# Kernel optimization log

Measured on AMD Instinct MI355X. Metric: run time of the kernel, lower is better.

The kernel has to match this reference:

```python
import jax, jax.numpy as jnp
import numpy as np

H = 512     # LSTM_HIDDEN_SIZE
IN = 64     # LSTM_INPUT_SIZE
B = 256
T = 512
OUT = 96    # output_size (decode horizon)


def setup_inputs() -> dict:
    key = jax.random.key(0)
    ks = jax.random.split(key, 32)
    k = 1.0 / np.sqrt(H)
    u = lambda kk, shape: jax.random.uniform(kk, shape, jnp.float32, -k, k)
    inp = {"inputs": jax.random.normal(ks[0], (B, T, IN), jnp.float32)}
    shapes = {
        "enc_Wih0": (4 * H, IN), "enc_Whh0": (4 * H, H), "enc_bih0": (4 * H,), "enc_bhh0": (4 * H,),
        "enc_Wih1": (4 * H, H),  "enc_Whh1": (4 * H, H), "enc_bih1": (4 * H,), "enc_bhh1": (4 * H,),
        "dec_Wih0": (4 * H, 1),  "dec_Whh0": (4 * H, H), "dec_bih0": (4 * H,), "dec_bhh0": (4 * H,),
        "dec_Wih1": (4 * H, H),  "dec_Whh1": (4 * H, H), "dec_bih1": (4 * H,), "dec_bhh1": (4 * H,),
        "proj_W": (1, H), "proj_b": (1,),
    }
    for i, (name, sh) in enumerate(shapes.items()):
        inp[name] = u(ks[i + 1], sh)
    inp["output_size"] = OUT
    return inp


def lstm_cell(x, h, c, Wih, Whh, bih, bhh):
    # PyTorch gate order: i, f, g, o
    z = x @ Wih.T + h @ Whh.T + (bih + bhh)
    i, f, g, o = jnp.split(z, 4, axis=-1)
    c_new = jax.nn.sigmoid(f) * c + jax.nn.sigmoid(i) * jnp.tanh(g)
    h_new = jax.nn.sigmoid(o) * jnp.tanh(c_new)
    return h_new, c_new


def reference(inputs,
              enc_Wih0, enc_Whh0, enc_bih0, enc_bhh0,
              enc_Wih1, enc_Whh1, enc_bih1, enc_bhh1,
              dec_Wih0, dec_Whh0, dec_bih0, dec_bhh0,
              dec_Wih1, dec_Whh1, dec_bih1, dec_bhh1,
              proj_W, proj_b, output_size):
    bsz = inputs.shape[0]
    hdim = enc_Whh0.shape[1]
    z = jnp.zeros((bsz, hdim), inputs.dtype)

    # ---- encoder: 2-layer LSTM over time (batch_first -> time-major scan) ----
    def enc_step(carry, x_t):
        h0, c0, h1, c1 = carry
        h0, c0 = lstm_cell(x_t, h0, c0, enc_Wih0, enc_Whh0, enc_bih0, enc_bhh0)
        h1, c1 = lstm_cell(h0, h1, c1, enc_Wih1, enc_Whh1, enc_bih1, enc_bhh1)
        return (h0, c0, h1, c1), None

    xs = jnp.swapaxes(inputs, 0, 1)  # [T, B, IN]
    (h0, c0, h1, c1), _ = jax.lax.scan(enc_step, (z, z, z, z), xs)

    def dec_step(carry, _):
        h0, c0, h1, c1, x = carry  # x: [B, 1]
        h0, c0 = lstm_cell(x, h0, c0, dec_Wih0, dec_Whh0, dec_bih0, dec_bhh0)
        h1, c1 = lstm_cell(h0, h1, c1, dec_Wih1, dec_Whh1, dec_bih1, dec_bhh1)
        y = h1 @ proj_W.T + proj_b  # [B, 1]
        return (h0, c0, h1, c1, y), y

    x0 = jnp.zeros((bsz, 1), inputs.dtype)
    _, ys = jax.lax.scan(dec_step, (h0, c0, h1, c1, x0), None, length=output_size)
    # ys: [OUT, B, 1] -> [B, OUT, 1]
    return jnp.swapaxes(ys, 0, 1)
```

## Files before the change

kernel.cpp:

```cpp
#include <hip/hip_runtime.h>
#include <math.h>

#define Bb   256
#define Tt   512
#define INn  64
#define Hh   512
#define OUTn 96
#define TPB  512
#define SP   (Hh*Bb)
#define RSTRIDE 36
#define HDR  12288

struct Params {
  const float *Xt;
  float *H0, *H1;
  unsigned int *flags;
  unsigned int *rel;
  const float *Wih0,*Whh0,*bih0,*bhh0,*Wih1,*Whh1,*bih1,*bhh1;
  const float *dWih0,*dWhh0,*dbih0,*dbhh0,*dWih1,*dWhh1,*dbih1,*dbhh1;
  const float *projW,*projb;
  float *out;
};

__device__ __forceinline__ float sigm(float x){ return 1.0f/(1.0f + expf(-x)); }

__device__ __forceinline__ void gridbar(unsigned int* flags, unsigned int* rel,
                                        unsigned int g, int nwg) {
  __syncthreads();
  const int tid = threadIdx.x;
  if (blockIdx.x == 0) {
    if (tid > 0 && tid < nwg) {
      while (__hip_atomic_load(&flags[tid*16], __ATOMIC_RELAXED, __HIP_MEMORY_SCOPE_AGENT) < g)
        __builtin_amdgcn_s_sleep(1);
    }
    __syncthreads();
    if (tid == 0) {
      __threadfence();
      __hip_atomic_store(rel, g, __ATOMIC_RELEASE, __HIP_MEMORY_SCOPE_AGENT);
    }
    __syncthreads();
  } else {
    if (tid == 0) {
      __threadfence();
      __hip_atomic_store(&flags[blockIdx.x*16], g, __ATOMIC_RELEASE, __HIP_MEMORY_SCOPE_AGENT);
      while (__hip_atomic_load(rel, __ATOMIC_RELAXED, __HIP_MEMORY_SCOPE_AGENT) < g)
        __builtin_amdgcn_s_sleep(1);
      __threadfence();
    }
    __syncthreads();
  }
}

__global__ void __launch_bounds__(256) xpose(const float* __restrict__ X, float* __restrict__ Xt) {
  __shared__ float tile[64][65];
  const int t = blockIdx.x;
  const int l = threadIdx.x & 63;
  const int r = threadIdx.x >> 6;
  for (int qd = 0; qd < 4; ++qd) {
    #pragma unroll
    for (int rep = 0; rep < 16; ++rep) {
      int bl = rep*4 + r;
      tile[bl][l] = X[(size_t)(qd*64 + bl)*(Tt*INn) + (size_t)t*INn + l];
    }
    __syncthreads();
    #pragma unroll
    for (int rep = 0; rep < 16; ++rep) {
      int i = rep*4 + r;
      Xt[(size_t)t*(INn*Bb) + (size_t)i*Bb + qd*64 + l] = tile[l][i];
    }
    __syncthreads();
  }
}

#define BFLY4(a)                                                   \
  do { _Pragma("unroll")                                           \
    for (int m_ = 0; m_ < 4; ++m_) {                               \
      a[m_] += __shfl_xor(a[m_], 8, 64);                           \
      a[m_] += __shfl_xor(a[m_], 16, 64);                          \
      a[m_] += __shfl_xor(a[m_], 32, 64);                          \
    } } while (0)

__global__ void __launch_bounds__(TPB, 4) lstm512(Params P) {
  __shared__ float WA[512][20];
  __shared__ float WB[512][8];
  __shared__ float WX[64][8];
  __shared__ float BS[16];
  __shared__ float PW[Hh];
  __shared__ float WXD[8];
  __shared__ float PBs;

  const int tid  = threadIdx.x;
  const int lane = tid & 63;
  const int kh   = lane >> 3;
  const int bqlo = lane & 7;
  const int bqhi = (tid >> 6) & 3;
  const int h    = tid >> 8;
  const int bq   = bqhi*8 + bqlo;
  const int uw   = blockIdx.x >> 1;
  const int bh   = blockIdx.x & 1;
  const int j    = 2*uw + h;
  const int h8   = h*8, h4 = h*4;
  const int boff = 128*bh + 4*bq;
  unsigned int bgen = 1;

  for (int e = tid; e < 512*16; e += TPB) {
    int k = e >> 4, c = e & 15, hh = c >> 3, s = c & 7;
    int unit = 2*uw + hh;
    WA[k][c] = (s < 4) ? P.Wih1[(size_t)(s*Hh + unit)*Hh + k]
                       : P.Whh0[(size_t)((s-4)*Hh + unit)*Hh + k];
  }
  for (int e = tid; e < 512*8; e += TPB) {
    int k = e >> 3, c = e & 7, hh = c >> 2, g = c & 3;
    WB[k][c] = P.Whh1[(size_t)(g*Hh + 2*uw + hh)*Hh + k];
  }
  for (int e = tid; e < 64*8; e += TPB) {
    int k = e >> 3, c = e & 7, hh = c >> 2, g = c & 3;
    WX[k][c] = P.Wih0[(size_t)(g*Hh + 2*uw + hh)*INn + k];
  }
  if (tid < 16) {
    int c = tid, hh = c >> 3, s = c & 7;
    int unit = 2*uw + hh;
    BS[c] = (s < 4) ? (P.bih1[s*Hh+unit] + P.bhh1[s*Hh+unit])
                    : (P.bih0[(s-4)*Hh+unit] + P.bhh0[(s-4)*Hh+unit]);
  }
  __syncthreads();

  float c0[4] = {0,0,0,0}, c1[4] = {0,0,0,0};

  for (int p = -1; p <= 511; ++p) {
    float z1i[4], z1f[4], z1g[4], z1o[4];
    float z0i[4], z0f[4], z0g[4], z0o[4];
    #pragma unroll
    for (int m = 0; m < 4; ++m) {
      z1i[m] = (kh==0) ? BS[h8+0] : 0.f; z1f[m] = (kh==0) ? BS[h8+1] : 0.f;
      z1g[m] = (kh==0) ? BS[h8+2] : 0.f; z1o[m] = (kh==0) ? BS[h8+3] : 0.f;
      z0i[m] = (kh==0) ? BS[h8+4] : 0.f; z0f[m] = (kh==0) ? BS[h8+5] : 0.f;
      z0g[m] = (kh==0) ? BS[h8+6] : 0.f; z0o[m] = (kh==0) ? BS[h8+7] : 0.f;
    }
    const float* __restrict__ h0in = P.H0 + (size_t)(p & 1)*SP + boff;
    const float* __restrict__ h1in = P.H1 + (size_t)((p+1) & 1)*SP + boff;
    #pragma unroll 4
    for (int kk = 0; kk < 64; ++kk) {
      const int k = kk*8 + kh;
      const float4 w1 = *reinterpret_cast<const float4*>(&WA[k][h8]);
      const float4 w0 = *reinterpret_cast<const float4*>(&WA[k][h8+4]);
      const float4 wb = *reinterpret_cast<const float4*>(&WB[k][h4]);
      const float4 hv4 = *reinterpret_cast<const float4*>(&h0in[k*Bb]);
      const float4 gv4 = *reinterpret_cast<const float4*>(&h1in[k*Bb]);
      const float* hv = &hv4.x;
      const float* gv = &gv4.x;
      #pragma unroll
      for (int m = 0; m < 4; ++m) {
        z1i[m]=fmaf(w1.x,hv[m],z1i[m]); z1f[m]=fmaf(w1.y,hv[m],z1f[m]);
        z1g[m]=fmaf(w1.z,hv[m],z1g[m]); z1o[m]=fmaf(w1.w,hv[m],z1o[m]);
        z0i[m]=fmaf(w0.x,hv[m],z0i[m]); z0f[m]=fmaf(w0.y,hv[m],z0f[m]);
        z0g[m]=fmaf(w0.z,hv[m],z0g[m]); z0o[m]=fmaf(w0.w,hv[m],z0o[m]);
        z1i[m]=fmaf(wb.x,gv[m],z1i[m]); z1f[m]=fmaf(wb.y,gv[m],z1f[m]);
        z1g[m]=fmaf(wb.z,gv[m],z1g[m]); z1o[m]=fmaf(wb.w,gv[m],z1o[m]);
      }
    }
    {
      int tx = (p+1 < Tt) ? (p+1) : (Tt-1);
      const float* __restrict__ xin = P.Xt + (size_t)tx*(INn*Bb) + boff;
      #pragma unroll
      for (int kk = 0; kk < 8; ++kk) {
        const int k = kk*8 + kh;
        const float4 wv = *reinterpret_cast<const float4*>(&WX[k][h4]);
        const float4 xv4 = *reinterpret_cast<const float4*>(&xin[k*Bb]);
        const float* xv = &xv4.x;
        #pragma unroll
        for (int m = 0; m < 4; ++m) {
          z0i[m]=fmaf(wv.x,xv[m],z0i[m]); z0f[m]=fmaf(wv.y,xv[m],z0f[m]);
          z0g[m]=fmaf(wv.z,xv[m],z0g[m]); z0o[m]=fmaf(wv.w,xv[m],z0o[m]);
        }
      }
    }
    BFLY4(z1i); BFLY4(z1f); BFLY4(z1g); BFLY4(z1o);
    BFLY4(z0i); BFLY4(z0f); BFLY4(z0g); BFLY4(z0o);

    if (p >= 0) {
      float4 o; float* ov = &o.x;
      #pragma unroll
      for (int m = 0; m < 4; ++m) {
        c1[m] = sigm(z1f[m])*c1[m] + sigm(z1i[m])*tanhf(z1g[m]);
        ov[m] = sigm(z1o[m])*tanhf(c1[m]);
      }
      if (kh == 0)
        *reinterpret_cast<float4*>(P.H1 + (size_t)(p & 1)*SP + (size_t)j*Bb + boff) = o;
    }
    if (p < 511) {
      float4 o; float* ov = &o.x;
      #pragma unroll
      for (int m = 0; m < 4; ++m) {
        c0[m] = sigm(z0f[m])*c0[m] + sigm(z0i[m])*tanhf(z0o[m]*0.f + z0g[m]);
        ov[m] = sigm(z0o[m])*tanhf(c0[m]);
      }
      if (kh == 0)
        *reinterpret_cast<float4*>(P.H0 + (size_t)((p+1) & 1)*SP + (size_t)j*Bb + boff) = o;
    }
    gridbar(P.flags, P.rel, bgen, 512); ++bgen;
  }

  for (int e = tid; e < 512*16; e += TPB) {
    int k = e >> 4, c = e & 15, hh = c >> 3, s = c & 7;
    int unit = 2*uw + hh;
    WA[k][c] = (s < 4) ? P.dWih1[(size_t)(s*Hh + unit)*Hh + k]
                       : P.dWhh1[(size_t)((s-4)*Hh + unit)*Hh + k];
  }
  for (int e = tid; e < 512*8; e += TPB) {
    int k = e >> 3, c = e & 7, hh = c >> 2, g = c & 3;
    WB[k][c] = P.dWhh0[(size_t)(g*Hh + 2*uw + hh)*Hh + k];
  }
  if (tid < 8) {
    int c = tid, hh = c >> 2, g = c & 3;
    WXD[c] = P.dWih0[g*Hh + 2*uw + hh];
  }
  if (tid >= 16 && tid < 32) {
    int c = tid - 16, hh = c >> 3, s = c & 7;
    int unit = 2*uw + hh;
    BS[c] = (s < 4) ? (P.dbih1[s*Hh+unit] + P.dbhh1[s*Hh+unit])
                    : (P.dbih0[(s-4)*Hh+unit] + P.dbhh0[(s-4)*Hh+unit]);
  }
  for (int k = tid; k < Hh; k += TPB) PW[k] = P.projW[k];
  if (tid == 0) PBs = P.projb[0];
  __syncthreads();

  for (int q = 0; q < OUTn; ++q) {
    float xq[4] = {0,0,0,0};
    if (q > 0) {
      const float* __restrict__ h1p = P.H1 + (size_t)((q+1)&1)*SP + boff;
      float acc[4] = {0,0,0,0};
      #pragma unroll 4
      for (int kk = 0; kk < 64; ++kk) {
        const int k = kk*8 + kh;
        float pw = PW[k];
        const float4 hp4 = *reinterpret_cast<const float4*>(&h1p[k*Bb]);
        const float* hp = &hp4.x;
        #pragma unroll
        for (int m = 0; m < 4; ++m) acc[m] = fmaf(pw, hp[m], acc[m]);
      }
      BFLY4(acc);
      #pragma unroll
      for (int m = 0; m < 4; ++m) xq[m] = acc[m] + PBs;
      if (uw == 0 && h == 0 && kh == 0) {
        #pragma unroll
        for (int m = 0; m < 4; ++m) P.out[(size_t)(boff + m)*OUTn + (q-1)] = xq[m];
      }
    }
    float zdi[4], zdf[4], zdg[4], zdo[4];
    #pragma unroll
    for (int m = 0; m < 4; ++m) {
      zdi[m] = (kh==0) ? BS[h8+4] : 0.f; zdf[m] = (kh==0) ? BS[h8+5] : 0.f;
      zdg[m] = (kh==0) ? BS[h8+6] : 0.f; zdo[m] = (kh==0) ? BS[h8+7] : 0.f;
    }
    {
      const float* __restrict__ h0p = P.H0 + (size_t)((q+1)&1)*SP + boff;
      #pragma unroll 4
      for (int kk = 0; kk < 64; ++kk) {
        const int k = kk*8 + kh;
        const float4 wv = *reinterpret_cast<const float4*>(&WB[k][h4]);
        const float4 hv4 = *reinterpret_cast<const float4*>(&h0p[k*Bb]);
        const float* hv = &hv4.x;
        #pragma unroll
        for (int m = 0; m < 4; ++m) {
          zdi[m]=fmaf(wv.x,hv[m],zdi[m]); zdf[m]=fmaf(wv.y,hv[m],zdf[m]);
          zdg[m]=fmaf(wv.z,hv[m],zdg[m]); zdo[m]=fmaf(wv.w,hv[m],zdo[m]);
        }
      }
    }
    BFLY4(zdi); BFLY4(zdf); BFLY4(zdg); BFLY4(zdo);
    {
      float4 o; float* ov = &o.x;
      #pragma unroll
      for (int m = 0; m < 4; ++m) {
        float zi = fmaf(WXD[h4+0], xq[m], zdi[m]);
        float zf = fmaf(WXD[h4+1], xq[m], zdf[m]);
        float zg = fmaf(WXD[h4+2], xq[m], zdg[m]);
        float zo = fmaf(WXD[h4+3], xq[m], zdo[m]);
        c0[m] = sigm(zf)*c0[m] + sigm(zi)*tanhf(zg);
        ov[m] = sigm(zo)*tanhf(c0[m]);
      }
      if (kh == 0)
        *reinterpret_cast<float4*>(P.H0 + (size_t)(q&1)*SP + (size_t)j*Bb + boff) = o;
    }
    gridbar(P.flags, P.rel, bgen, 512); ++bgen;

    float yi[4], yf[4], yg[4], yo[4];
    #pragma unroll
    for (int m = 0; m < 4; ++m) {
      yi[m] = (kh==0) ? BS[h8+0] : 0.f; yf[m] = (kh==0) ? BS[h8+1] : 0.f;
      yg[m] = (kh==0) ? BS[h8+2] : 0.f; yo[m] = (kh==0) ? BS[h8+3] : 0.f;
    }
    {
      const float* __restrict__ h0c = P.H0 + (size_t)(q&1)*SP + boff;
      const float* __restrict__ h1q = P.H1 + (size_t)((q+1)&1)*SP + boff;
      #pragma unroll 4
      for (int kk = 0; kk < 64; ++kk) {
        const int k = kk*8 + kh;
        const float4 w1 = *reinterpret_cast<const float4*>(&WA[k][h8]);
        const float4 w2 = *reinterpret_cast<const float4*>(&WA[k][h8+4]);
        const float4 av4 = *reinterpret_cast<const float4*>(&h0c[k*Bb]);
        const float4 dv4 = *reinterpret_cast<const float4*>(&h1q[k*Bb]);
        const float* av = &av4.x;
        const float* dv = &dv4.x;
        #pragma unroll
        for (int m = 0; m < 4; ++m) {
          yi[m]=fmaf(w1.x,av[m],yi[m]); yf[m]=fmaf(w1.y,av[m],yf[m]);
          yg[m]=fmaf(w1.z,av[m],yg[m]); yo[m]=fmaf(w1.w,av[m],yo[m]);
          yi[m]=fmaf(w2.x,dv[m],yi[m]); yf[m]=fmaf(w2.y,dv[m],yf[m]);
          yg[m]=fmaf(w2.z,dv[m],yg[m]); yo[m]=fmaf(w2.w,dv[m],yo[m]);
        }
      }
    }
    BFLY4(yi); BFLY4(yf); BFLY4(yg); BFLY4(yo);
    {
      float4 o; float* ov = &o.x;
      #pragma unroll
      for (int m = 0; m < 4; ++m) {
        c1[m] = sigm(yf[m])*c1[m] + sigm(yi[m])*tanhf(yg[m]);
        ov[m] = sigm(yo[m])*tanhf(c1[m]);
      }
      if (kh == 0)
        *reinterpret_cast<float4*>(P.H1 + (size_t)(q&1)*SP + (size_t)j*Bb + boff) = o;
    }
    gridbar(P.flags, P.rel, bgen, 512); ++bgen;
  }

  if (uw == 0 && h == 0) {
    const float* __restrict__ h1f = P.H1 + (size_t)((OUTn-1)&1)*SP + boff;
    float acc[4] = {0,0,0,0};
    #pragma unroll 4
    for (int kk = 0; kk < 64; ++kk) {
      const int k = kk*8 + kh;
      float pw = PW[k];
      const float4 hp4 = *reinterpret_cast<const float4*>(&h1f[k*Bb]);
      const float* hp = &hp4.x;
      #pragma unroll
      for (int m = 0; m < 4; ++m) acc[m] = fmaf(pw, hp[m], acc[m]);
    }
    BFLY4(acc);
    if (kh == 0) {
      #pragma unroll
      for (int m = 0; m < 4; ++m)
        P.out[(size_t)(boff + m)*OUTn + (OUTn-1)] = acc[m] + PBs;
    }
  }
}

__global__ void __launch_bounds__(TPB, 2) lstm_fb(Params P) {
  __shared__ float WA[512][32];
  __shared__ float WB[512][16];
  __shared__ float WX[64][16];
  __shared__ float BS[32];
  __shared__ float PW[Hh];
  __shared__ float WXD[16];
  __shared__ float PBs;
  __shared__ float RED[2][128][RSTRIDE];

  const int tid = threadIdx.x;
  const int w   = blockIdx.x;
  const int uw  = w >> 1;
  const int bh  = w & 1;
  const int bq  = tid & 31;
  const int h   = (tid >> 5) & 3;
  const int kh  = tid >> 7;
  const int j   = 4*uw + h;
  const int h8  = h*8, h4 = h*4;
  const int slot = h*32 + bq;
  const int boff = 128*bh + 4*bq;
  unsigned int bgen = 1;

  for (int e = tid; e < 512*32; e += TPB) {
    int k = e >> 5, c = e & 31, hh = c >> 3, s = c & 7;
    int unit = 4*uw + hh;
    WA[k][c] = (s < 4) ? P.Wih1[(size_t)(s*Hh + unit)*Hh + k]
                       : P.Whh0[(size_t)((s-4)*Hh + unit)*Hh + k];
  }
  for (int e = tid; e < 512*16; e += TPB) {
    int k = e >> 4, c = e & 15, hh = c >> 2, g = c & 3;
    WB[k][c] = P.Whh1[(size_t)(g*Hh + 4*uw + hh)*Hh + k];
  }
  for (int e = tid; e < 64*16; e += TPB) {
    int k = e >> 4, c = e & 15, hh = c >> 2, g = c & 3;
    WX[k][c] = P.Wih0[(size_t)(g*Hh + 4*uw + hh)*INn + k];
  }
  if (tid < 32) {
    int c = tid, hh = c >> 3, s = c & 7;
    int unit = 4*uw + hh;
    BS[c] = (s < 4) ? (P.bih1[s*Hh+unit] + P.bhh1[s*Hh+unit])
                    : (P.bih0[(s-4)*Hh+unit] + P.bhh0[(s-4)*Hh+unit]);
  }
  __syncthreads();

  float c0[4] = {0,0,0,0}, c1[4] = {0,0,0,0};
  float4 eA_h[4], eA_g[4], eB_h[4], eB_g[4];

#define ENC_LOAD(HB, GB, K0)                                              \
  _Pragma("unroll")                                                       \
  for (int t = 0; t < 4; ++t) {                                           \
    HB[t] = *reinterpret_cast<const float4*>(&h0in[((K0)+t)*Bb]);         \
    GB[t] = *reinterpret_cast<const float4*>(&h1in[((K0)+t)*Bb]);         \
  }
#define ENC_COMPUTE(HB, GB, K0)                                           \
  _Pragma("unroll")                                                       \
  for (int t = 0; t < 4; ++t) {                                           \
    const int k = (K0) + t;                                               \
    const float4 w1 = *reinterpret_cast<const float4*>(&WA[k][h8]);       \
    const float4 w0 = *reinterpret_cast<const float4*>(&WA[k][h8+4]);     \
    const float4 wb = *reinterpret_cast<const float4*>(&WB[k][h4]);       \
    const float* hv = &HB[t].x;                                           \
    const float* gv = &GB[t].x;                                           \
    _Pragma("unroll")                                                     \
    for (int m = 0; m < 4; ++m) {                                         \
      z1i[m]=fmaf(w1.x,hv[m],z1i[m]); z1f[m]=fmaf(w1.y,hv[m],z1f[m]);     \
      z1g[m]=fmaf(w1.z,hv[m],z1g[m]); z1o[m]=fmaf(w1.w,hv[m],z1o[m]);     \
      z0i[m]=fmaf(w0.x,hv[m],z0i[m]); z0f[m]=fmaf(w0.y,hv[m],z0f[m]);     \
      z0g[m]=fmaf(w0.z,hv[m],z0g[m]); z0o[m]=fmaf(w0.w,hv[m],z0o[m]);     \
      z1i[m]=fmaf(wb.x,gv[m],z1i[m]); z1f[m]=fmaf(wb.y,gv[m],z1f[m]);     \
      z1g[m]=fmaf(wb.z,gv[m],z1g[m]); z1o[m]=fmaf(wb.w,gv[m],z1o[m]);     \
    }                                                                     \
  }

  for (int p = -1; p <= 511; ++p) {
    float z1i[4], z1f[4], z1g[4], z1o[4];
    float z0i[4], z0f[4], z0g[4], z0o[4];
    #pragma unroll
    for (int m = 0; m < 4; ++m) {
      z1i[m] = (kh==0) ? BS[h8+0] : 0.f; z1f[m] = (kh==0) ? BS[h8+1] : 0.f;
      z1g[m] = (kh==0) ? BS[h8+2] : 0.f; z1o[m] = (kh==0) ? BS[h8+3] : 0.f;
      z0i[m] = (kh==0) ? BS[h8+4] : 0.f; z0f[m] = (kh==0) ? BS[h8+5] : 0.f;
      z0g[m] = (kh==0) ? BS[h8+6] : 0.f; z0o[m] = (kh==0) ? BS[h8+7] : 0.f;
    }
    const float* __restrict__ h0in = P.H0 + (size_t)(p & 1)*SP + boff;
    const float* __restrict__ h1in = P.H1 + (size_t)((p+1) & 1)*SP + boff;
    const int kb = kh*128, ke = kb + 128;

    ENC_LOAD(eA_h, eA_g, kb);
    {
      int tx = (p+1 < Tt) ? (p+1) : (Tt-1);
      const float* __restrict__ xin = P.Xt + (size_t)tx*(INn*Bb) + boff;
      #pragma unroll 4
      for (int k = kh*16; k < kh*16 + 16; ++k) {
        const float4 wv = *reinterpret_cast<const float4*>(&WX[k][h4]);
        const float4 xv4 = *reinterpret_cast<const float4*>(&xin[k*Bb]);
        const float* xv = &xv4.x;
        #pragma unroll
        for (int m = 0; m < 4; ++m) {
          z0i[m]=fmaf(wv.x,xv[m],z0i[m]); z0f[m]=fmaf(wv.y,xv[m],z0f[m]);
          z0g[m]=fmaf(wv.z,xv[m],z0g[m]); z0o[m]=fmaf(wv.w,xv[m],z0o[m]);
        }
      }
    }
    for (int kk = kb; kk < ke; kk += 8) {
      ENC_LOAD(eB_h, eB_g, kk+4);
      ENC_COMPUTE(eA_h, eA_g, kk);
      const int kn = (kk+8 < ke) ? (kk+8) : kb;
      ENC_LOAD(eA_h, eA_g, kn);
      ENC_COMPUTE(eB_h, eB_g, kk+4);
    }

    if (kh >= 2) {
      float* r = &RED[kh-2][slot][0];
      *reinterpret_cast<float4*>(&r[ 0]) = make_float4(z1i[0],z1i[1],z1i[2],z1i[3]);
      *reinterpret_cast<float4*>(&r[ 4]) = make_float4(z1f[0],z1f[1],z1f[2],z1f[3]);
      *reinterpret_cast<float4*>(&r[ 8]) = make_float4(z1g[0],z1g[1],z1g[2],z1g[3]);
      *reinterpret_cast<float4*>(&r[12]) = make_float4(z1o[0],z1o[1],z1o[2],z1o[3]);
      *reinterpret_cast<float4*>(&r[16]) = make_float4(z0i[0],z0i[1],z0i[2],z0i[3]);
      *reinterpret_cast<float4*>(&r[20]) = make_float4(z0f[0],z0f[1],z0f[2],z0f[3]);
      *reinterpret_cast<float4*>(&r[24]) = make_float4(z0g[0],z0g[1],z0g[2],z0g[3]);
      *reinterpret_cast<float4*>(&r[28]) = make_float4(z0o[0],z0o[1],z0o[2],z0o[3]);
    }
    __syncthreads();
    if (kh < 2) {
      float* r = &RED[kh][slot][0];
      {
        const float* rr = r;
        #pragma unroll
        for (int m = 0; m < 4; ++m) {
          z1i[m]+=rr[ 0+m]; z1f[m]+=rr[ 4+m]; z1g[m]+=rr[ 8+m]; z1o[m]+=rr[12+m];
          z0i[m]+=rr[16+m]; z0f[m]+=rr[20+m]; z0g[m]+=rr[24+m]; z0o[m]+=rr[28+m];
        }
      }
      if (kh == 1) {
        *reinterpret_cast<float4*>(&r[ 0]) = make_float4(z1i[0],z1i[1],z1i[2],z1i[3]);
        *reinterpret_cast<float4*>(&r[ 4]) = make_float4(z1f[0],z1f[1],z1f[2],z1f[3]);
        *reinterpret_cast<float4*>(&r[ 8]) = make_float4(z1g[0],z1g[1],z1g[2],z1g[3]);
        *reinterpret_cast<float4*>(&r[12]) = make_float4(z1o[0],z1o[1],z1o[2],z1o[3]);
        *reinterpret_cast<float4*>(&r[16]) = make_float4(z0i[0],z0i[1],z0i[2],z0i[3]);
        *reinterpret_cast<float4*>(&r[20]) = make_float4(z0f[0],z0f[1],z0f[2],z0f[3]);
        *reinterpret_cast<float4*>(&r[24]) = make_float4(z0g[0],z0g[1],z0g[2],z0g[3]);
        *reinterpret_cast<float4*>(&r[28]) = make_float4(z0o[0],z0o[1],z0o[2],z0o[3]);
      }
    }
    __syncthreads();
    if (kh == 0) {
      const float* rr = &RED[1][slot][0];
      #pragma unroll
      for (int m = 0; m < 4; ++m) {
        z1i[m]+=rr[ 0+m]; z1f[m]+=rr[ 4+m]; z1g[m]+=rr[ 8+m]; z1o[m]+=rr[12+m];
        z0i[m]+=rr[16+m]; z0f[m]+=rr[20+m]; z0g[m]+=rr[24+m]; z0o[m]+=rr[28+m];
      }
      if (p >= 0) {
        float* st = P.H1 + (size_t)(p & 1)*SP + (size_t)j*Bb + boff;
        float4 o; float* ov = &o.x;
        #pragma unroll
        for (int m = 0; m < 4; ++m) {
          c1[m] = sigm(z1f[m])*c1[m] + sigm(z1i[m])*tanhf(z1g[m]);
          ov[m] = sigm(z1o[m])*tanhf(c1[m]);
        }
        *reinterpret_cast<float4*>(st) = o;
      }
      if (p < 511) {
        float* st = P.H0 + (size_t)((p+1) & 1)*SP + (size_t)j*Bb + boff;
        float4 o; float* ov = &o.x;
        #pragma unroll
        for (int m = 0; m < 4; ++m) {
          c0[m] = sigm(z0f[m])*c0[m] + sigm(z0i[m])*tanhf(z0g[m]);
          ov[m] = sigm(z0o[m])*tanhf(c0[m]);
        }
        *reinterpret_cast<float4*>(st) = o;
      }
    }
    gridbar(P.flags, P.rel, bgen, 256); ++bgen;
  }

  for (int e = tid; e < 512*32; e += TPB) {
    int k = e >> 5, c = e & 31, hh = c >> 3, s = c & 7;
    int unit = 4*uw + hh;
    WA[k][c] = (s < 4) ? P.dWih1[(size_t)(s*Hh + unit)*Hh + k]
                       : P.dWhh1[(size_t)((s-4)*Hh + unit)*Hh + k];
  }
  for (int e = tid; e < 512*16; e += TPB) {
    int k = e >> 4, c = e & 15, hh = c >> 2, g = c & 3;
    WB[k][c] = P.dWhh0[(size_t)(g*Hh + 4*uw + hh)*Hh + k];
  }
  if (tid < 16) {
    int c = tid, hh = c >> 2, g = c & 3;
    WXD[c] = P.dWih0[g*Hh + 4*uw + hh];
  }
  if (tid >= 32 && tid < 64) {
    int c = tid - 32, hh = c >> 3, s = c & 7;
    int unit = 4*uw + hh;
    BS[c] = (s < 4) ? (P.dbih1[s*Hh+unit] + P.dbhh1[s*Hh+unit])
                    : (P.dbih0[(s-4)*Hh+unit] + P.dbhh0[(s-4)*Hh+unit]);
  }
  for (int k = tid; k < Hh; k += TPB) PW[k] = P.projW[k];
  if (tid == 0) PBs = P.projb[0];
  __syncthreads();

  for (int q = 0; q < OUTn; ++q) {
    float xq[4];
    #pragma unroll
    for (int m = 0; m < 4; ++m) xq[m] = (kh==0 && q>0) ? PBs : 0.f;
    if (q > 0) {
      const float* __restrict__ h1p = P.H1 + (size_t)((q+1)&1)*SP + boff;
      const int kb = kh*128, ke = kb + 128;
      #pragma unroll 4
      for (int k = kb; k < ke; ++k) {
        float pw = PW[k];
        const float4 hp4 = *reinterpret_cast<const float4*>(&h1p[k*Bb]);
        const float* hp = &hp4.x;
        #pragma unroll
        for (int m = 0; m < 4; ++m) xq[m] = fmaf(pw, hp[m], xq[m]);
      }
    }
    float zd[4][4];
    #pragma unroll
    for (int g = 0; g < 4; ++g)
      #pragma unroll
      for (int m = 0; m < 4; ++m)
        zd[g][m] = (kh==0) ? BS[h8+4+g] : 0.f;
    {
      const float* __restrict__ h0p = P.H0 + (size_t)((q+1)&1)*SP + boff;
      const int kb = kh*128, ke = kb + 128;
      #pragma unroll 4
      for (int k = kb; k < ke; ++k) {
        const float4 wv = *reinterpret_cast<const float4*>(&WB[k][h4]);
        const float4 hv4 = *reinterpret_cast<const float4*>(&h0p[k*Bb]);
        const float* hv = &hv4.x;
        #pragma unroll
        for (int m = 0; m < 4; ++m) {
          zd[0][m]=fmaf(wv.x,hv[m],zd[0][m]); zd[1][m]=fmaf(wv.y,hv[m],zd[1][m]);
          zd[2][m]=fmaf(wv.z,hv[m],zd[2][m]); zd[3][m]=fmaf(wv.w,hv[m],zd[3][m]);
        }
      }
    }
    if (kh >= 2) {
      float* r = &RED[kh-2][slot][0];
      #pragma unroll
      for (int g = 0; g < 4; ++g)
        *reinterpret_cast<float4*>(&r[g*4]) = make_float4(zd[g][0],zd[g][1],zd[g][2],zd[g][3]);
      *reinterpret_cast<float4*>(&r[16]) = make_float4(xq[0],xq[1],xq[2],xq[3]);
    }
    __syncthreads();
    if (kh < 2) {
      float* r = &RED[kh][slot][0];
      #pragma unroll
      for (int g = 0; g < 4; ++g) {
        const float4 v = *reinterpret_cast<const float4*>(&r[g*4]);
        zd[g][0]+=v.x; zd[g][1]+=v.y; zd[g][2]+=v.z; zd[g][3]+=v.w;
      }
      {
        const float4 v = *reinterpret_cast<const float4*>(&r[16]);
        xq[0]+=v.x; xq[1]+=v.y; xq[2]+=v.z; xq[3]+=v.w;
      }
      if (kh == 1) {
        #pragma unroll
        for (int g = 0; g < 4; ++g)
          *reinterpret_cast<float4*>(&r[g*4]) = make_float4(zd[g][0],zd[g][1],zd[g][2],zd[g][3]);
        *reinterpret_cast<float4*>(&r[16]) = make_float4(xq[0],xq[1],xq[2],xq[3]);
      }
    }
    __syncthreads();
    if (kh == 0) {
      const float* r = &RED[1][slot][0];
      #pragma unroll
      for (int g = 0; g < 4; ++g) {
        const float4 v = *reinterpret_cast<const float4*>(&r[g*4]);
        zd[g][0]+=v.x; zd[g][1]+=v.y; zd[g][2]+=v.z; zd[g][3]+=v.w;
      }
      {
        const float4 v = *reinterpret_cast<const float4*>(&r[16]);
        xq[0]+=v.x; xq[1]+=v.y; xq[2]+=v.z; xq[3]+=v.w;
      }
      if (uw == 0 && h == 0 && q > 0) {
        #pragma unroll
        for (int m = 0; m < 4; ++m) P.out[(size_t)(boff + m)*OUTn + (q-1)] = xq[m];
      }
      float* st = P.H0 + (size_t)(q&1)*SP + (size_t)j*Bb + boff;
      float4 o; float* ov = &o.x;
      #pragma unroll
      for (int m = 0; m < 4; ++m) {
        float zi = fmaf(WXD[h4+0], xq[m], zd[0][m]);
        float zf = fmaf(WXD[h4+1], xq[m], zd[1][m]);
        float zg = fmaf(WXD[h4+2], xq[m], zd[2][m]);
        float zo = fmaf(WXD[h4+3], xq[m], zd[3][m]);
        c0[m] = sigm(zf)*c0[m] + sigm(zi)*tanhf(zg);
        ov[m] = sigm(zo)*tanhf(c0[m]);
      }
      *reinterpret_cast<float4*>(st) = o;
    }
    gridbar(P.flags, P.rel, bgen, 256); ++bgen;

    float y[4][4];
    #pragma unroll
    for (int g = 0; g < 4; ++g)
      #pragma unroll
      for (int m = 0; m < 4; ++m)
        y[g][m] = (kh==0) ? BS[h8+g] : 0.f;
    {
      const float* __restrict__ h0c = P.H0 + (size_t)(q&1)*SP + boff;
      const float* __restrict__ h1q = P.H1 + (size_t)((q+1)&1)*SP + boff;
      const int kb = kh*128, ke = kb + 128;
      #pragma unroll 4
      for (int k = kb; k < ke; ++k) {
        const float4 w1 = *reinterpret_cast<const float4*>(&WA[k][h8]);
        const float4 w2 = *reinterpret_cast<const float4*>(&WA[k][h8+4]);
        const float4 av4 = *reinterpret_cast<const float4*>(&h0c[k*Bb]);
        const float4 dv4 = *reinterpret_cast<const float4*>(&h1q[k*Bb]);
        const float* av = &av4.x;
        const float* dv = &dv4.x;
        #pragma unroll
        for (int m = 0; m < 4; ++m) {
          y[0][m]=fmaf(w1.x,av[m],y[0][m]); y[1][m]=fmaf(w1.y,av[m],y[1][m]);
          y[2][m]=fmaf(w1.z,av[m],y[2][m]); y[3][m]=fmaf(w1.w,av[m],y[3][m]);
          y[0][m]=fmaf(w2.x,dv[m],y[0][m]); y[1][m]=fmaf(w2.y,dv[m],y[1][m]);
          y[2][m]=fmaf(w2.z,dv[m],y[2][m]); y[3][m]=fmaf(w2.w,dv[m],y[3][m]);
        }
      }
    }
    if (kh >= 2) {
      float* r = &RED[kh-2][slot][0];
      #pragma unroll
      for (int g = 0; g < 4; ++g)
        *reinterpret_cast<float4*>(&r[g*4]) = make_float4(y[g][0],y[g][1],y[g][2],y[g][3]);
    }
    __syncthreads();
    if (kh < 2) {
      float* r = &RED[kh][slot][0];
      #pragma unroll
      for (int g = 0; g < 4; ++g) {
        const float4 v = *reinterpret_cast<const float4*>(&r[g*4]);
        y[g][0]+=v.x; y[g][1]+=v.y; y[g][2]+=v.z; y[g][3]+=v.w;
      }
      if (kh == 1) {
        #pragma unroll
        for (int g = 0; g < 4; ++g)
          *reinterpret_cast<float4*>(&r[g*4]) = make_float4(y[g][0],y[g][1],y[g][2],y[g][3]);
      }
    }
    __syncthreads();
    if (kh == 0) {
      const float* r = &RED[1][slot][0];
      #pragma unroll
      for (int g = 0; g < 4; ++g) {
        const float4 v = *reinterpret_cast<const float4*>(&r[g*4]);
        y[g][0]+=v.x; y[g][1]+=v.y; y[g][2]+=v.z; y[g][3]+=v.w;
      }
      float* st = P.H1 + (size_t)(q&1)*SP + (size_t)j*Bb + boff;
      float4 o; float* ov = &o.x;
      #pragma unroll
      for (int m = 0; m < 4; ++m) {
        c1[m] = sigm(y[1][m])*c1[m] + sigm(y[0][m])*tanhf(y[2][m]);
        ov[m] = sigm(y[3][m])*tanhf(c1[m]);
      }
      *reinterpret_cast<float4*>(st) = o;
    }
    gridbar(P.flags, P.rel, bgen, 256); ++bgen;
  }

  if (kh == 0 && uw == 0 && h == 0) {
    const float* __restrict__ h1f = P.H1 + (size_t)((OUTn-1)&1)*SP + boff;
    float acc[4] = {PBs, PBs, PBs, PBs};
    #pragma unroll 4
    for (int k = 0; k < Hh; ++k) {
      float pw = PW[k];
      const float4 hp4 = *reinterpret_cast<const float4*>(&h1f[k*Bb]);
      const float* hp = &hp4.x;
      #pragma unroll
      for (int m = 0; m < 4; ++m) acc[m] = fmaf(pw, hp[m], acc[m]);
    }
    #pragma unroll
    for (int m = 0; m < 4; ++m) P.out[(size_t)(boff + m)*OUTn + (OUTn-1)] = acc[m];
  }
}

extern "C" void kernel_launch(void* const* d_in, const int* in_sizes, int n_in,
                              void* d_out, int out_size, void* d_ws, size_t ws_size,
                              hipStream_t stream) {
  Params P;
  const float* X = (const float*)d_in[0];
  P.Wih0  = (const float*)d_in[1];  P.Whh0  = (const float*)d_in[2];
  P.bih0  = (const float*)d_in[3];  P.bhh0  = (const float*)d_in[4];
  P.Wih1  = (const float*)d_in[5];  P.Whh1  = (const float*)d_in[6];
  P.bih1  = (const float*)d_in[7];  P.bhh1  = (const float*)d_in[8];
  P.dWih0 = (const float*)d_in[9];  P.dWhh0 = (const float*)d_in[10];
  P.dbih0 = (const float*)d_in[11]; P.dbhh0 = (const float*)d_in[12];
  P.dWih1 = (const float*)d_in[13]; P.dWhh1 = (const float*)d_in[14];
  P.dbih1 = (const float*)d_in[15]; P.dbhh1 = (const float*)d_in[16];
  P.projW = (const float*)d_in[17]; P.projb = (const float*)d_in[18];

  float* ws = (float*)d_ws;
  P.flags = (unsigned int*)ws;
  P.rel   = (unsigned int*)ws + 8192;
  P.H0  = ws + HDR;
  P.H1  = ws + HDR + 2*SP;
  float* Xt = ws + HDR + 4*SP;
  P.Xt  = Xt;
  P.out = (float*)d_out;

  hipMemsetAsync(d_ws, 0, (size_t)(HDR + 4*SP)*sizeof(float), stream);
  hipLaunchKernelGGL(xpose, dim3(Tt), dim3(256), 0, stream, X, Xt);

  void* args[] = { &P };
  int occ = 0;
  hipError_t qe = hipOccupancyMaxActiveBlocksPerMultiprocessor(
      &occ, (const void*)lstm512, TPB, 0);
  if (qe == hipSuccess && occ >= 2) {
    hipError_t le = hipLaunchCooperativeKernel((void*)lstm512, dim3(512), dim3(TPB), args, 0, stream);
    if (le != hipSuccess) {
      (void)hipGetLastError();
      hipLaunchKernelGGL(lstm512, dim3(512), dim3(TPB), 0, stream, P);
    }
  } else {
    (void)hipGetLastError();
    hipLaunchCooperativeKernel((void*)lstm_fb, dim3(256), dim3(TPB), args, 0, stream);
  }
}
```

Baseline: 25.91 ms.

## Split grid barrier into two independent batch-half groups

After: 26.33 ms. No clear change (+1.6%).

```diff
diff --git a/kernel.cpp b/kernel.cpp
--- a/kernel.cpp
+++ b/kernel.cpp
@@ -24,26 +24,29 @@
 
 __device__ __forceinline__ float sigm(float x){ return 1.0f/(1.0f + expf(-x)); }
 
-__device__ __forceinline__ void gridbar(unsigned int* flags, unsigned int* rel,
-                                        unsigned int g, int nwg) {
+template<int NR>
+__device__ __forceinline__ void gridbar_g(unsigned int* flags, unsigned int* rel,
+                                          unsigned int g, int bh, int rank) {
   __syncthreads();
   const int tid = threadIdx.x;
-  if (blockIdx.x == 0) {
-    if (tid > 0 && tid < nwg) {
-      while (__hip_atomic_load(&flags[tid*16], __ATOMIC_RELAXED, __HIP_MEMORY_SCOPE_AGENT) < g)
+  unsigned int* gflags = flags + bh*4096;
+  unsigned int* grel   = rel   + bh*64;
+  if (rank == 0) {
+    if (tid > 0 && tid < NR) {
+      while (__hip_atomic_load(&gflags[tid*16], __ATOMIC_RELAXED, __HIP_MEMORY_SCOPE_AGENT) < g)
         __builtin_amdgcn_s_sleep(1);
     }
     __syncthreads();
     if (tid == 0) {
       __threadfence();
-      __hip_atomic_store(rel, g, __ATOMIC_RELEASE, __HIP_MEMORY_SCOPE_AGENT);
+      __hip_atomic_store(grel, g, __ATOMIC_RELEASE, __HIP_MEMORY_SCOPE_AGENT);
     }
     __syncthreads();
   } else {
     if (tid == 0) {
       __threadfence();
-      __hip_atomic_store(&flags[blockIdx.x*16], g, __ATOMIC_RELEASE, __HIP_MEMORY_SCOPE_AGENT);
-      while (__hip_atomic_load(rel, __ATOMIC_RELAXED, __HIP_MEMORY_SCOPE_AGENT) < g)
+      __hip_atomic_store(&gflags[rank*16], g, __ATOMIC_RELEASE, __HIP_MEMORY_SCOPE_AGENT);
+      while (__hip_atomic_load(grel, __ATOMIC_RELAXED, __HIP_MEMORY_SCOPE_AGENT) < g)
         __builtin_amdgcn_s_sleep(1);
       __threadfence();
     }
@@ -80,7 +83,7 @@
       a[m_] += __shfl_xor(a[m_], 32, 64);                          \
     } } while (0)
 
-__global__ void __launch_bounds__(TPB, 4) lstm512(Params P) {
+__global__ void __launch_bounds__(TPB, 4) lstm512g(Params P) {
   __shared__ float WA[512][20];
   __shared__ float WB[512][8];
   __shared__ float WX[64][8];
@@ -96,8 +99,9 @@
   const int bqhi = (tid >> 6) & 3;
   const int h    = tid >> 8;
   const int bq   = bqhi*8 + bqlo;
-  const int uw   = blockIdx.x >> 1;
-  const int bh   = blockIdx.x & 1;
+  const int w    = blockIdx.x;
+  const int bh   = w >> 8;
+  const int uw   = w & 255;
   const int j    = 2*uw + h;
   const int h8   = h*8, h4 = h*4;
   const int boff = 128*bh + 4*bq;
@@ -192,13 +196,13 @@
       float4 o; float* ov = &o.x;
       #pragma unroll
       for (int m = 0; m < 4; ++m) {
-        c0[m] = sigm(z0f[m])*c0[m] + sigm(z0i[m])*tanhf(z0o[m]*0.f + z0g[m]);
+        c0[m] = sigm(z0f[m])*c0[m] + sigm(z0i[m])*tanhf(z0g[m]);
         ov[m] = sigm(z0o[m])*tanhf(c0[m]);
       }
       if (kh == 0)
         *reinterpret_cast<float4*>(P.H0 + (size_t)((p+1) & 1)*SP + (size_t)j*Bb + boff) = o;
     }
-    gridbar(P.flags, P.rel, bgen, 512); ++bgen;
+    gridbar_g<256>(P.flags, P.rel, bgen, bh, uw); ++bgen;
   }
 
   for (int e = tid; e < 512*16; e += TPB) {
@@ -283,7 +287,7 @@
       if (kh == 0)
         *reinterpret_cast<float4*>(P.H0 + (size_t)(q&1)*SP + (size_t)j*Bb + boff) = o;
     }
-    gridbar(P.flags, P.rel, bgen, 512); ++bgen;
+    gridbar_g<256>(P.flags, P.rel, bgen, bh, uw); ++bgen;
 
     float yi[4], yf[4], yg[4], yo[4];
     #pragma unroll
@@ -323,7 +327,7 @@
       if (kh == 0)
         *reinterpret_cast<float4*>(P.H1 + (size_t)(q&1)*SP + (size_t)j*Bb + boff) = o;
     }
-    gridbar(P.flags, P.rel, bgen, 512); ++bgen;
+    gridbar_g<256>(P.flags, P.rel, bgen, bh, uw); ++bgen;
   }
 
   if (uw == 0 && h == 0) {
@@ -521,7 +525,7 @@
         *reinterpret_cast<float4*>(st) = o;
       }
     }
-    gridbar(P.flags, P.rel, bgen, 256); ++bgen;
+    gridbar_g<128>(P.flags, P.rel, bgen, bh, uw); ++bgen;
   }
 
   for (int e = tid; e < 512*32; e += TPB) {
@@ -640,7 +644,7 @@
       }
       *reinterpret_cast<float4*>(st) = o;
     }
-    gridbar(P.flags, P.rel, bgen, 256); ++bgen;
+    gridbar_g<128>(P.flags, P.rel, bgen, bh, uw); ++bgen;
 
     float y[4][4];
     #pragma unroll
@@ -706,7 +710,7 @@
       }
       *reinterpret_cast<float4*>(st) = o;
     }
-    gridbar(P.flags, P.rel, bgen, 256); ++bgen;
+    gridbar_g<128>(P.flags, P.rel, bgen, bh, uw); ++bgen;
   }
 
   if (kh == 0 && uw == 0 && h == 0) {
@@ -732,8 +736,9 @@
   const float* X = (const float*)d_in[0];
   P.Wih0  = (const float*)d_in[1];  P.Whh0  = (const float*)d_in[2];
   P.bih0  = (const float*)d_in[3];  P.bhh0  = (const float*)d_in[4];
+  P.bih1  = (const float*)d_in[7];
   P.Wih1  = (const float*)d_in[5];  P.Whh1  = (const float*)d_in[6];
-  P.bih1  = (const float*)d_in[7];  P.bhh1  = (const float*)d_in[8];
+  P.bhh1  = (const float*)d_in[8];
   P.dWih0 = (const float*)d_in[9];  P.dWhh0 = (const float*)d_in[10];
   P.dbih0 = (const float*)d_in[11]; P.dbhh0 = (const float*)d_in[12];
   P.dWih1 = (const float*)d_in[13]; P.dWhh1 = (const float*)d_in[14];
@@ -755,12 +760,12 @@
   void* args[] = { &P };
   int occ = 0;
   hipError_t qe = hipOccupancyMaxActiveBlocksPerMultiprocessor(
-      &occ, (const void*)lstm512, TPB, 0);
+      &occ, (const void*)lstm512g, TPB, 0);
   if (qe == hipSuccess && occ >= 2) {
-    hipError_t le = hipLaunchCooperativeKernel((void*)lstm512, dim3(512), dim3(TPB), args, 0, stream);
+    hipError_t le = hipLaunchCooperativeKernel((void*)lstm512g, dim3(512), dim3(TPB), args, 0, stream);
     if (le != hipSuccess) {
       (void)hipGetLastError();
-      hipLaunchKernelGGL(lstm512, dim3(512), dim3(TPB), 0, stream, P);
+      hipLaunchKernelGGL(lstm512g, dim3(512), dim3(TPB), 0, stream, P);
     }
   } else {
     (void)hipGetLastError();
```
